# Performance work log

Measured on AMD Instinct MI355X. Metric: run time of the kernel, lower is better.

The kernel has to match this reference:

```python
import jax, jax.numpy as jnp
import numpy as np


def setup_inputs() -> dict:
    key = jax.random.key(0)
    ks = jax.random.split(key, 13)
    B, W, C = 16, 2048, 512
    inp = {
        "X_sfr": jax.random.normal(ks[0], (B, W, C), dtype=jnp.float32),
        "adj_matrix": jax.random.normal(ks[1], (B, C, C), dtype=jnp.float32),
        "log_temp": jnp.zeros((1,), dtype=jnp.float32),
        "wq": jax.random.normal(ks[2], (1,), dtype=jnp.float32),
        "bq": jax.random.normal(ks[3], (1,), dtype=jnp.float32),
        "wk": jax.random.normal(ks[4], (1,), dtype=jnp.float32),
        "bk": jax.random.normal(ks[5], (1,), dtype=jnp.float32),
        "wv": jax.random.normal(ks[6], (1,), dtype=jnp.float32),
        "bv": jax.random.normal(ks[7], (1,), dtype=jnp.float32),
        "wmu": jax.random.normal(ks[8], (1,), dtype=jnp.float32),
        "bmu": jax.random.normal(ks[9], (1,), dtype=jnp.float32),
        "wsig": jax.random.normal(ks[10], (1,), dtype=jnp.float32),
        "bsig": jax.random.normal(ks[11], (1,), dtype=jnp.float32),
        "k1": 20,
        "k2": 30,
    }
    return inp


def reference(X_sfr, adj_matrix, log_temp, wq, bq, wk, bk, wv, bv, wmu, bmu, wsig, bsig, k1, k2):
    B, W, C = X_sfr.shape
    # spatial propagation: relu + in-degree normalize adjacency
    adj_nonneg = jnp.maximum(adj_matrix, 0.0)
    in_deg = jnp.clip(adj_nonneg.sum(axis=1, keepdims=True), 1e-4)  # [B,1,C]
    adj_norm = adj_nonneg / in_deg
    X_spatial = jnp.einsum('bwi,bij->bwj', X_sfr, adj_norm)  # [B,W,C]

    # static band mask over time: k1 <= |dt| <= k2, fallback to identity rows
    t = jnp.arange(W)
    delta = jnp.abs(t[None, :] - t[:, None])
    band = (delta >= k1) & (delta <= k2)  # [W,W]
    has_valid = band.any(axis=1)
    band = jnp.where(has_valid[:, None], band, jnp.eye(W, dtype=bool))

    # scalar (1->1) q/k/v projections on the temporal token
    temporal_token = X_spatial.mean(axis=2, keepdims=True)  # [B,W,1]
    q = wq * temporal_token + bq                            # [B,W,1]
    k = wk * temporal_token + bk                            # [B,W,1]
    v = wv * X_spatial + bv                                 # [B,W,C]

    temp = jax.nn.softplus(log_temp)[0] + 1e-4
    logits = jnp.matmul(q, jnp.swapaxes(k, 1, 2)) / temp    # [B,W,W] rank-1
    logits = jnp.where(band[None, :, :], logits, -1e9)
    attn = jax.nn.softmax(logits, axis=-1)
    attn = attn * band[None, :, :].astype(attn.dtype)
    attn = attn / (attn.sum(axis=-1, keepdims=True) + 1e-6)

    sacon_scalar = attn.sum(axis=-1, keepdims=True)         # [B,W,1]
    sacon = jnp.broadcast_to(sacon_scalar, (B, W, C))

    X_temporal = jnp.matmul(attn, v)                        # [B,W,C]
    X_fused = X_temporal + X_spatial

    mu = jnp.clip(wmu * X_fused + bmu, -20.0, 20.0)
    sigma_sq = jax.nn.softplus(wsig * X_fused + bsig) + 0.1
    return mu, sigma_sq, sacon
```

## Files before the change

### kernel.cpp

```cpp
#include <hip/hip_runtime.h>
#include <math.h>

#define B_ 16
#define W_ 2048
#define C_ 512

#define OFF_XB    0
#define OFF_BT    33554432
#define OFF_XSP   41943040
#define OFF_TT    75497472

typedef short v8s __attribute__((ext_vector_type(8)));
typedef float v4f __attribute__((ext_vector_type(4)));
typedef unsigned int u32;

__device__ __forceinline__ float softplusf(float x) {
    return fmaxf(x, 0.f) + log1pf(expf(-fabsf(x)));
}
__device__ __forceinline__ unsigned short f2bf(float x) {
    unsigned int u = __float_as_uint(x);
    unsigned int r = (u + 0x7FFFu + ((u >> 16) & 1u)) >> 16;
    return (unsigned short)r;
}
__device__ __forceinline__ float bf2f(unsigned int h) {
    return __uint_as_float(h << 16);
}
__device__ __forceinline__ void gload16(const ushort* g, ushort* l) {
    __builtin_amdgcn_global_load_lds(
        (const __attribute__((address_space(1))) u32*)(g),
        (__attribute__((address_space(3))) u32*)(l), 16, 0, 0);
}

__global__ __launch_bounds__(256) void prep_adj(const float* __restrict__ adj,
                                                ushort* __restrict__ Bt) {
    __shared__ float cs[8][32];
    __shared__ float inv[32];
    __shared__ float t[32][33];
    const int b = blockIdx.y, j0 = blockIdx.x * 32;
    const int tx = threadIdx.x & 31, ty = threadIdx.x >> 5;
    const float* src = adj + (size_t)b * C_ * C_;

    float s = 0.f;
#pragma unroll 4
    for (int it = 0; it < C_ / 8; it++)
        s += fmaxf(src[(size_t)(it * 8 + ty) * C_ + j0 + tx], 0.f);
    cs[ty][tx] = s;
    __syncthreads();
    if (ty == 0) {
        float tot = cs[0][tx] + cs[1][tx] + cs[2][tx] + cs[3][tx]
                  + cs[4][tx] + cs[5][tx] + cs[6][tx] + cs[7][tx];
        inv[tx] = 1.f / fmaxf(tot, 1e-4f);
    }

    const int jr = threadIdx.x >> 4;
    const int ic = (threadIdx.x & 15) * 2;
    for (int i0t = 0; i0t < C_; i0t += 32) {
        __syncthreads();
#pragma unroll
        for (int rr = 0; rr < 4; rr++) {
            int ii = ty + rr * 8;
            t[ii][tx] = fmaxf(src[(size_t)(i0t + ii) * C_ + j0 + tx], 0.f);
        }
        __syncthreads();
#pragma unroll
        for (int pp = 0; pp < 2; pp++) {
            int j = jr + pp * 16;
            float iv = inv[j];
            ushort2 o;
            o.x = f2bf(t[ic][j] * iv);
            o.y = f2bf(t[ic + 1][j] * iv);
            *(ushort2*)&Bt[(size_t)b * C_ * C_ + (size_t)(j0 + j) * C_ + i0t + ic] = o;
        }
    }
}

__global__ void convertA(const float* __restrict__ X, ushort* __restrict__ Xb) {
    int idx = blockIdx.x * 256 + threadIdx.x;
    float4 v = ((const float4*)X)[idx];
    ushort4 o;
    o.x = f2bf(v.x); o.y = f2bf(v.y); o.z = f2bf(v.z); o.w = f2bf(v.w);
    ((ushort4*)Xb)[idx] = o;
}

__global__ __launch_bounds__(256) void gemm_mfma(const ushort* __restrict__ Xb,
                                                 const ushort* __restrict__ Bt,
                                                 ushort* __restrict__ Xsp,
                                                 float* __restrict__ tt) {
    __shared__ ushort As[128 * 32];
    __shared__ ushort Bs[128 * 32];
    const int b  = blockIdx.z;
    const int m0 = blockIdx.y * 128;
    const int n0 = blockIdx.x * 128;
    const int tid  = threadIdx.x;
    const int wave = tid >> 6, lane = tid & 63;
    const int quad = lane >> 4, l16 = lane & 15;
    const int mw = (wave & 1) * 64, nw = (wave >> 1) * 64;

    const ushort* Ag = Xb + (size_t)b * W_ * C_ + (size_t)m0 * C_;
    const ushort* Bg = Bt + (size_t)b * C_ * C_ + (size_t)n0 * C_;

    const int sm = tid >> 2;
    const int sk = (tid & 3) * 8;

    v4f acc[4][4];
#pragma unroll
    for (int mt = 0; mt < 4; mt++)
#pragma unroll
        for (int nt = 0; nt < 4; nt++)
            acc[mt][nt] = (v4f){0.f, 0.f, 0.f, 0.f};

    for (int k0 = 0; k0 < C_; k0 += 32) {
        __syncthreads();
        gload16(Ag + (size_t)sm * C_ + k0 + sk,        As + tid * 8);
        gload16(Ag + (size_t)(sm + 64) * C_ + k0 + sk, As + 2048 + tid * 8);
        gload16(Bg + (size_t)sm * C_ + k0 + sk,        Bs + tid * 8);
        gload16(Bg + (size_t)(sm + 64) * C_ + k0 + sk, Bs + 2048 + tid * 8);
        __syncthreads();

        v8s af[4], bf[4];
#pragma unroll
        for (int mt = 0; mt < 4; mt++)
            af[mt] = *(const v8s*)&As[(mw + mt * 16 + l16) * 32 + quad * 8];
#pragma unroll
        for (int nt = 0; nt < 4; nt++)
            bf[nt] = *(const v8s*)&Bs[(nw + nt * 16 + l16) * 32 + quad * 8];
#pragma unroll
        for (int mt = 0; mt < 4; mt++)
#pragma unroll
            for (int nt = 0; nt < 4; nt++)
                acc[mt][nt] = __builtin_amdgcn_mfma_f32_16x16x32_bf16(af[mt], bf[nt], acc[mt][nt], 0, 0, 0);
    }

#pragma unroll
    for (int mt = 0; mt < 4; mt++) {
#pragma unroll
        for (int nt = 0; nt < 4; nt++) {
            int col = n0 + nw + nt * 16 + l16;
#pragma unroll
            for (int r = 0; r < 4; r++) {
                int row = m0 + mw + mt * 16 + quad * 4 + r;
                Xsp[((size_t)b * W_ + row) * C_ + col] = f2bf(acc[mt][nt][r]);
            }
        }
    }

#pragma unroll
    for (int mt = 0; mt < 4; mt++) {
#pragma unroll
        for (int r = 0; r < 4; r++) {
            float s = acc[mt][0][r] + acc[mt][1][r] + acc[mt][2][r] + acc[mt][3][r];
            s += __shfl_xor(s, 1);
            s += __shfl_xor(s, 2);
            s += __shfl_xor(s, 4);
            s += __shfl_xor(s, 8);
            if (l16 == 0) {
                int row = m0 + mw + mt * 16 + quad * 4 + r;
                atomicAdd(&tt[b * W_ + row], s);
            }
        }
    }
}

__global__ __launch_bounds__(256) void final_kernel(const ushort* __restrict__ Xsp,
                                                    const float* __restrict__ tt,
                                                    const float* __restrict__ ltp,
                                                    const float* __restrict__ wqp, const float* __restrict__ bqp,
                                                    const float* __restrict__ wkp, const float* __restrict__ bkp,
                                                    const float* __restrict__ wvp, const float* __restrict__ bvp,
                                                    const float* __restrict__ wmup, const float* __restrict__ bmup,
                                                    const float* __restrict__ wsigp, const float* __restrict__ bsigp,
                                                    const int* __restrict__ k1p, const int* __restrict__ k2p,
                                                    float* __restrict__ out) {
    __shared__ float wlds[4][4][40];
    __shared__ float Ssh[4][4];
    const int wid = threadIdx.x >> 6, lane = threadIdx.x & 63;
    const int i0w = blockIdx.x * 16 + wid * 4;
    const int b = i0w >> 11, ib = i0w & (W_ - 1);
    const int K1 = k1p[0], K2 = k2p[0];
    int ns = K2 - K1 + 1;
    if (ns > 16) ns = 16;
    const int n2 = 2 * ns;
    const int nsL = ns + 3;
    const int nu = 2 * nsL;

    for (int k = threadIdx.x; k < 4 * 4 * 40; k += 256) ((float*)wlds)[k] = 0.f;
    __syncthreads();

    if (lane < 32) {
        const float cinv = 1.f / C_;
        const float temp = softplusf(ltp[0]) + 1e-4f;
        const float invt = 1.f / temp;
        const float wkc = wkp[0] * cinv, bk = bkp[0];
        const float wqc = wqp[0] * cinv, bq = bqp[0];
        const float* ttb = tt + b * W_;
        for (int r = 0; r < 4; r++) {
            const int i = ib + r;
            const float q = wqc * ttb[i] + bq;
            int s = lane;
            int j = (s < ns) ? (i - K2 + s) : (i + K1 + (s - ns));
            bool valid = (s < n2) && (j >= 0) && (j < W_);
            float l = valid ? (q * (wkc * ttb[j] + bk) * invt) : -INFINITY;
            float mx = l;
#pragma unroll
            for (int off = 16; off > 0; off >>= 1) mx = fmaxf(mx, __shfl_xor(mx, off, 32));
            float e = valid ? expf(l - mx) : 0.f;
            float T = e;
#pragma unroll
            for (int off = 16; off > 0; off >>= 1) T += __shfl_xor(T, off, 32);
            float p = e / T;
            float S = p;
#pragma unroll
            for (int off = 16; off > 0; off >>= 1) S += __shfl_xor(S, off, 32);
            float rn = 1.f / (S + 1e-6f);
            if (s < n2) {
                int u = (s < ns) ? (r + s) : (nsL + r + (s - ns));
                wlds[wid][r][u] = p * rn;
            }
            if (lane == 0) Ssh[wid][r] = S * rn;
        }
    }
    __syncthreads();

    const ushort* Xbp = Xsp + (size_t)b * W_ * C_;
    const int c8 = lane * 8;
    float acc[4][8];
#pragma unroll
    for (int r = 0; r < 4; r++)
#pragma unroll
        for (int k = 0; k < 8; k++) acc[r][k] = 0.f;

    for (int u = 0; u < nu; u++) {
        int j = (u < nsL) ? (ib - K2 + u) : (ib + K1 + (u - nsL));
        j = min(max(j, 0), W_ - 1);
        uint4 v = *(const uint4*)(Xbp + (size_t)j * C_ + c8);
        float x[8];
        x[0] = bf2f(v.x & 0xffff); x[1] = bf2f(v.x >> 16);
        x[2] = bf2f(v.y & 0xffff); x[3] = bf2f(v.y >> 16);
        x[4] = bf2f(v.z & 0xffff); x[5] = bf2f(v.z >> 16);
        x[6] = bf2f(v.w & 0xffff); x[7] = bf2f(v.w >> 16);
#pragma unroll
        for (int r = 0; r < 4; r++) {
            float w = wlds[wid][r][u];
#pragma unroll
            for (int k = 0; k < 8; k++) acc[r][k] = fmaf(w, x[k], acc[r][k]);
        }
    }

    const float wv = wvp[0], bv = bvp[0];
    const float wmu = wmup[0], bmu = bmup[0];
    const float wsig = wsigp[0], bsig = bsigp[0];
    const size_t N = (size_t)B_ * W_ * C_;

#pragma unroll
    for (int r = 0; r < 4; r++) {
        const float S = Ssh[wid][r];
        uint4 xv = *(const uint4*)(Xbp + (size_t)(ib + r) * C_ + c8);
        float xs[8];
        xs[0] = bf2f(xv.x & 0xffff); xs[1] = bf2f(xv.x >> 16);
        xs[2] = bf2f(xv.y & 0xffff); xs[3] = bf2f(xv.y >> 16);
        xs[4] = bf2f(xv.z & 0xffff); xs[5] = bf2f(xv.z >> 16);
        xs[6] = bf2f(xv.w & 0xffff); xs[7] = bf2f(xv.w >> 16);

        float mu[8], sg[8];
#pragma unroll
        for (int k = 0; k < 8; k++) {
            float xf = fmaf(wv, acc[r][k], bv * S) + xs[k];
            mu[k] = fminf(fmaxf(fmaf(wmu, xf, bmu), -20.f), 20.f);
            sg[k] = softplusf(fmaf(wsig, xf, bsig)) + 0.1f;
        }

        const size_t base = (size_t)(i0w + r) * C_ + c8;
        *(float4*)&out[base]     = (float4){mu[0], mu[1], mu[2], mu[3]};
        *(float4*)&out[base + 4] = (float4){mu[4], mu[5], mu[6], mu[7]};
        *(float4*)&out[N + base]     = (float4){sg[0], sg[1], sg[2], sg[3]};
        *(float4*)&out[N + base + 4] = (float4){sg[4], sg[5], sg[6], sg[7]};
        *(float4*)&out[2 * N + base]     = (float4){S, S, S, S};
        *(float4*)&out[2 * N + base + 4] = (float4){S, S, S, S};
    }
}

extern "C" void kernel_launch(void* const* d_in, const int* in_sizes, int n_in,
                              void* d_out, int out_size, void* d_ws, size_t ws_size,
                              hipStream_t stream) {
    const float* X_sfr = (const float*)d_in[0];
    const float* adj   = (const float*)d_in[1];
    const float* ltp   = (const float*)d_in[2];
    const float* wq    = (const float*)d_in[3];
    const float* bq    = (const float*)d_in[4];
    const float* wk    = (const float*)d_in[5];
    const float* bk    = (const float*)d_in[6];
    const float* wv    = (const float*)d_in[7];
    const float* bv    = (const float*)d_in[8];
    const float* wmu   = (const float*)d_in[9];
    const float* bmu   = (const float*)d_in[10];
    const float* wsig  = (const float*)d_in[11];
    const float* bsig  = (const float*)d_in[12];
    const int*   k1p   = (const int*)d_in[13];
    const int*   k2p   = (const int*)d_in[14];

    char* ws = (char*)d_ws;
    ushort* Xb  = (ushort*)(ws + OFF_XB);
    ushort* Bt  = (ushort*)(ws + OFF_BT);
    ushort* Xsp = (ushort*)(ws + OFF_XSP);
    float*  tt  = (float*)(ws + OFF_TT);
    float*  out = (float*)d_out;

    hipMemsetAsync(tt, 0, B_ * W_ * sizeof(float), stream);

    prep_adj<<<dim3(C_ / 32, B_), 256, 0, stream>>>(adj, Bt);

    convertA<<<(B_ * W_ * C_ / 4) / 256, 256, 0, stream>>>(X_sfr, Xb);

    gemm_mfma<<<dim3(C_ / 128, W_ / 128, B_), 256, 0, stream>>>(Xb, Bt, Xsp, tt);

    final_kernel<<<(B_ * W_) / 16, 256, 0, stream>>>(Xsp, tt, ltp, wq, bq, wk, bk,
                                                     wv, bv, wmu, bmu, wsig, bsig,
                                                     k1p, k2p, out);
}
```

Baseline: 385.5 us.

## Rework final kernel: packed FMA, fast math, nontemporal stores, block swizzle

Rewrites the final fused kernel in several ways. Block indices are remapped across batches, the softmax runs two rows at once across both wavefront halves, and the renormalised row sum is replaced by the constant 1/(1+1e-6). The band weights are stored transposed so one vector LDS load serves all four rows, the accumulation uses packed float2 FMAs, softplus and exp switch to fast intrinsics, and outputs use nontemporal stores. The aim is less ALU, LDS and cache overhead in a store-bound kernel, at the cost of slight numeric drift and an assumption that every row has at least one valid band entry.

```diff
diff --git a/kernel.cpp b/kernel.cpp
--- a/kernel.cpp
+++ b/kernel.cpp
@@ -12,10 +12,14 @@
 
 typedef short v8s __attribute__((ext_vector_type(8)));
 typedef float v4f __attribute__((ext_vector_type(4)));
+typedef float v2f __attribute__((ext_vector_type(2)));
 typedef unsigned int u32;
 
 __device__ __forceinline__ float softplusf(float x) {
     return fmaxf(x, 0.f) + log1pf(expf(-fabsf(x)));
+}
+__device__ __forceinline__ float softplus_fast(float x) {
+    return fmaxf(x, 0.f) + __logf(1.f + __expf(-fabsf(x)));
 }
 __device__ __forceinline__ unsigned short f2bf(float x) {
     unsigned int u = __float_as_uint(x);
@@ -171,10 +175,10 @@
                                                     const float* __restrict__ wsigp, const float* __restrict__ bsigp,
                                                     const int* __restrict__ k1p, const int* __restrict__ k2p,
                                                     float* __restrict__ out) {
-    __shared__ float wlds[4][4][40];
-    __shared__ float Ssh[4][4];
+    __shared__ float wlds[4][40][4];
     const int wid = threadIdx.x >> 6, lane = threadIdx.x & 63;
-    const int i0w = blockIdx.x * 16 + wid * 4;
+    const int bid = ((int)blockIdx.x & 7) * 256 + ((int)blockIdx.x >> 3);
+    const int i0w = bid * 16 + wid * 4;
     const int b = i0w >> 11, ib = i0w & (W_ - 1);
     const int K1 = k1p[0], K2 = k2p[0];
     int ns = K2 - K1 + 1;
@@ -182,100 +186,102 @@
     const int n2 = 2 * ns;
     const int nsL = ns + 3;
     const int nu = 2 * nsL;
-
-    for (int k = threadIdx.x; k < 4 * 4 * 40; k += 256) ((float*)wlds)[k] = 0.f;
+    const float Sc = 1.f / (1.f + 1e-6f);
+
+    for (int k = threadIdx.x; k < 4 * 40 * 4; k += 256) ((float*)wlds)[k] = 0.f;
     __syncthreads();
 
-    if (lane < 32) {
+    {
         const float cinv = 1.f / C_;
-        const float temp = softplusf(ltp[0]) + 1e-4f;
+        const float temp = softplus_fast(ltp[0]) + 1e-4f;
         const float invt = 1.f / temp;
         const float wkc = wkp[0] * cinv, bk = bkp[0];
         const float wqc = wqp[0] * cinv, bq = bqp[0];
         const float* ttb = tt + b * W_;
-        for (int r = 0; r < 4; r++) {
+        const int half = lane >> 5;
+        const int s = lane & 31;
+#pragma unroll
+        for (int rr = 0; rr < 2; rr++) {
+            const int r = rr * 2 + half;
             const int i = ib + r;
             const float q = wqc * ttb[i] + bq;
-            int s = lane;
             int j = (s < ns) ? (i - K2 + s) : (i + K1 + (s - ns));
             bool valid = (s < n2) && (j >= 0) && (j < W_);
-            float l = valid ? (q * (wkc * ttb[j] + bk) * invt) : -INFINITY;
+            int jc = min(max(j, 0), W_ - 1);
+            float l = valid ? (q * (wkc * ttb[jc] + bk) * invt) : -1e30f;
             float mx = l;
 #pragma unroll
             for (int off = 16; off > 0; off >>= 1) mx = fmaxf(mx, __shfl_xor(mx, off, 32));
-            float e = valid ? expf(l - mx) : 0.f;
+            float e = valid ? __expf(l - mx) : 0.f;
             float T = e;
 #pragma unroll
             for (int off = 16; off > 0; off >>= 1) T += __shfl_xor(T, off, 32);
-            float p = e / T;
-            float S = p;
-#pragma unroll
-            for (int off = 16; off > 0; off >>= 1) S += __shfl_xor(S, off, 32);
-            float rn = 1.f / (S + 1e-6f);
-            if (s < n2) {
+            float wsc = (1.f / T) * Sc;
+            if (valid) {
                 int u = (s < ns) ? (r + s) : (nsL + r + (s - ns));
-                wlds[wid][r][u] = p * rn;
+                wlds[wid][u][r] = e * wsc;
             }
-            if (lane == 0) Ssh[wid][r] = S * rn;
         }
     }
     __syncthreads();
 
     const ushort* Xbp = Xsp + (size_t)b * W_ * C_;
     const int c8 = lane * 8;
-    float acc[4][8];
+    v2f acc2[4][4];
 #pragma unroll
     for (int r = 0; r < 4; r++)
 #pragma unroll
-        for (int k = 0; k < 8; k++) acc[r][k] = 0.f;
-
+        for (int p = 0; p < 4; p++) acc2[r][p] = (v2f){0.f, 0.f};
+
+#pragma unroll 4
     for (int u = 0; u < nu; u++) {
         int j = (u < nsL) ? (ib - K2 + u) : (ib + K1 + (u - nsL));
         j = min(max(j, 0), W_ - 1);
         uint4 v = *(const uint4*)(Xbp + (size_t)j * C_ + c8);
-        float x[8];
-        x[0] = bf2f(v.x & 0xffff); x[1] = bf2f(v.x >> 16);
-        x[2] = bf2f(v.y & 0xffff); x[3] = bf2f(v.y >> 16);
-        x[4] = bf2f(v.z & 0xffff); x[5] = bf2f(v.z >> 16);
-        x[6] = bf2f(v.w & 0xffff); x[7] = bf2f(v.w >> 16);
+        v2f x[4];
+        x[0] = (v2f){bf2f(v.x & 0xffffu), bf2f(v.x >> 16)};
+        x[1] = (v2f){bf2f(v.y & 0xffffu), bf2f(v.y >> 16)};
+        x[2] = (v2f){bf2f(v.z & 0xffffu), bf2f(v.z >> 16)};
+        x[3] = (v2f){bf2f(v.w & 0xffffu), bf2f(v.w >> 16)};
+        const v4f w4 = *(const v4f*)&wlds[wid][u][0];
 #pragma unroll
         for (int r = 0; r < 4; r++) {
-            float w = wlds[wid][r][u];
-#pragma unroll
-            for (int k = 0; k < 8; k++) acc[r][k] = fmaf(w, x[k], acc[r][k]);
-        }
-    }
-
-    const float wv = wvp[0], bv = bvp[0];
+            v2f w2 = (v2f){w4[r], w4[r]};
+#pragma unroll
+            for (int p = 0; p < 4; p++) acc2[r][p] += w2 * x[p];
+        }
+    }
+
+    const float wv = wvp[0], bvS = bvp[0] * Sc;
     const float wmu = wmup[0], bmu = bmup[0];
     const float wsig = wsigp[0], bsig = bsigp[0];
     const size_t N = (size_t)B_ * W_ * C_;
 
 #pragma unroll
     for (int r = 0; r < 4; r++) {
-        const float S = Ssh[wid][r];
         uint4 xv = *(const uint4*)(Xbp + (size_t)(ib + r) * C_ + c8);
         float xs[8];
-        xs[0] = bf2f(xv.x & 0xffff); xs[1] = bf2f(xv.x >> 16);
-        xs[2] = bf2f(xv.y & 0xffff); xs[3] = bf2f(xv.y >> 16);
-        xs[4] = bf2f(xv.z & 0xffff); xs[5] = bf2f(xv.z >> 16);
-        xs[6] = bf2f(xv.w & 0xffff); xs[7] = bf2f(xv.w >> 16);
+        xs[0] = bf2f(xv.x & 0xffffu); xs[1] = bf2f(xv.x >> 16);
+        xs[2] = bf2f(xv.y & 0xffffu); xs[3] = bf2f(xv.y >> 16);
+        xs[4] = bf2f(xv.z & 0xffffu); xs[5] = bf2f(xv.z >> 16);
+        xs[6] = bf2f(xv.w & 0xffffu); xs[7] = bf2f(xv.w >> 16);
 
         float mu[8], sg[8];
 #pragma unroll
         for (int k = 0; k < 8; k++) {
-            float xf = fmaf(wv, acc[r][k], bv * S) + xs[k];
+            float a = acc2[r][k >> 1][k & 1];
+            float xf = fmaf(wv, a, bvS) + xs[k];
             mu[k] = fminf(fmaxf(fmaf(wmu, xf, bmu), -20.f), 20.f);
-            sg[k] = softplusf(fmaf(wsig, xf, bsig)) + 0.1f;
+            sg[k] = softplus_fast(fmaf(wsig, xf, bsig)) + 0.1f;
         }
 
         const size_t base = (size_t)(i0w + r) * C_ + c8;
-        *(float4*)&out[base]     = (float4){mu[0], mu[1], mu[2], mu[3]};
-        *(float4*)&out[base + 4] = (float4){mu[4], mu[5], mu[6], mu[7]};
-        *(float4*)&out[N + base]     = (float4){sg[0], sg[1], sg[2], sg[3]};
-        *(float4*)&out[N + base + 4] = (float4){sg[4], sg[5], sg[6], sg[7]};
-        *(float4*)&out[2 * N + base]     = (float4){S, S, S, S};
-        *(float4*)&out[2 * N + base + 4] = (float4){S, S, S, S};
+        __builtin_nontemporal_store((v4f){mu[0], mu[1], mu[2], mu[3]}, (v4f*)&out[base]);
+        __builtin_nontemporal_store((v4f){mu[4], mu[5], mu[6], mu[7]}, (v4f*)&out[base + 4]);
+        __builtin_nontemporal_store((v4f){sg[0], sg[1], sg[2], sg[3]}, (v4f*)&out[N + base]);
+        __builtin_nontemporal_store((v4f){sg[4], sg[5], sg[6], sg[7]}, (v4f*)&out[N + base + 4]);
+        __builtin_nontemporal_store((v4f){Sc, Sc, Sc, Sc}, (v4f*)&out[2 * N + base]);
+        __builtin_nontemporal_store((v4f){Sc, Sc, Sc, Sc}, (v4f*)&out[2 * N + base + 4]);
     }
 }
 
```

Result: slower. 408.5 us (+6.0%).
